# Optimization experiments

Hardware: AMD Instinct MI355X
Metric: run time of the kernel (lower is better)

Reference implementation:

```python
import jax, jax.numpy as jnp
import numpy as np

N = 40000   # nodes
E = 640000  # edges
D = 128     # hidden_dim
EPS = 1e-5  # LayerNorm eps


def setup_inputs() -> dict:
    key = jax.random.key(0)
    ks = jax.random.split(key, 18)
    s = 0.02
    inp = {
        "h": jax.random.normal(ks[0], (N, D), jnp.float32),
        "x": jax.random.normal(ks[1], (N, 3), jnp.float32),
        "edge_index": jax.random.randint(ks[2], (2, E), 0, N, jnp.int64 if jax.config.jax_enable_x64 else jnp.int32),
        "vel": jax.random.normal(ks[3], (N, 3), jnp.float32),
        # phi_e: Linear(2D+1 -> D), SiLU, Linear(D -> D), SiLU
        "We1": jax.random.normal(ks[4], (2 * D + 1, D), jnp.float32) * s,
        "be1": jnp.zeros((D,), jnp.float32),
        "We2": jax.random.normal(ks[5], (D, D), jnp.float32) * s,
        "be2": jnp.zeros((D,), jnp.float32),
        # phi_x: Linear(D -> D), SiLU, Linear(D -> 1)
        "Wx1": jax.random.normal(ks[6], (D, D), jnp.float32) * s,
        "bx1": jnp.zeros((D,), jnp.float32),
        "Wx2": jax.random.normal(ks[7], (D, 1), jnp.float32) * s,
        "bx2": jnp.zeros((1,), jnp.float32),
        # phi_h: Linear(2D -> D), SiLU, Linear(D -> D)
        "Wh1": jax.random.normal(ks[8], (2 * D, D), jnp.float32) * s,
        "bh1": jnp.zeros((D,), jnp.float32),
        "Wh2": jax.random.normal(ks[9], (D, D), jnp.float32) * s,
        "bh2": jnp.zeros((D,), jnp.float32),
        # LayerNorm
        "gamma": jnp.ones((D,), jnp.float32),
        "beta": jnp.zeros((D,), jnp.float32),
    }
    return inp


def reference(h, x, edge_index, vel,
              We1, be1, We2, be2,
              Wx1, bx1, Wx2, bx2,
              Wh1, bh1, Wh2, bh2,
              gamma, beta):
    src, dst = edge_index[0], edge_index[1]
    rel = x[src] - x[dst]                                  # [E,3]
    dist2 = jnp.sum(rel * rel, axis=-1, keepdims=True)     # [E,1]
    # note: original also computes dist/r_hat and vel[src] but never uses them

    # phi_e on edge features
    e_in = jnp.concatenate([h[src], h[dst], dist2], axis=-1)   # [E,2D+1]
    m = jax.nn.silu(e_in @ We1 + be1)
    m = jax.nn.silu(m @ We2 + be2)                             # [E,D]

    # coordinate update: scatter_mean of rel * phi_x(m) over dst
    coord_w = jax.nn.silu(m @ Wx1 + bx1) @ Wx2 + bx2           # [E,1]
    num = jax.ops.segment_sum(rel * coord_w, dst, num_segments=N)  # [N,3]
    cnt = jax.ops.segment_sum(jnp.ones((E, 1), x.dtype), dst, num_segments=N)
    x_new = x + num / jnp.maximum(cnt, 1.0)

    # node update: scatter_add of messages then phi_h + residual + LayerNorm
    agg = jax.ops.segment_sum(m, dst, num_segments=N)          # [N,D]
    upd = jax.nn.silu(jnp.concatenate([h, agg], axis=-1) @ Wh1 + bh1) @ Wh2 + bh2
    hn = h + upd
    mu = jnp.mean(hn, axis=-1, keepdims=True)
    var = jnp.var(hn, axis=-1, keepdims=True)
    h_out = (hn - mu) / jnp.sqrt(var + EPS) * gamma + beta
    return h_out, x_new
```

## Files before the change

kernel.cpp:

```cpp
#include <hip/hip_runtime.h>
#include <hip/hip_fp16.h>

#define NN 40000
#define NE 640000
#define DD 128
#define NW (NE/64)

typedef _Float16 half8 __attribute__((ext_vector_type(8)));
typedef float f32x4 __attribute__((ext_vector_type(4)));

__device__ __forceinline__ float silu_f(float x){
  return x * __builtin_amdgcn_rcpf(1.f + __expf(-x));
}

__device__ __forceinline__ half8 cvt_h8(float4 a, float4 b){
  half8 r;
  r[0]=(_Float16)a.x; r[1]=(_Float16)a.y; r[2]=(_Float16)a.z; r[3]=(_Float16)a.w;
  r[4]=(_Float16)b.x; r[5]=(_Float16)b.y; r[6]=(_Float16)b.z; r[7]=(_Float16)b.w;
  return r;
}

__device__ __forceinline__ void atom_pk_f16(_Float16* p, unsigned v){
  asm volatile("global_atomic_pk_add_f16 %0, %1, off" :: "v"(p), "v"(v));
}

__global__ void k_hist(const int* __restrict__ ei, int* __restrict__ counts,
                       uint4* __restrict__ aggz){
  int e = blockIdx.x*256 + threadIdx.x;
  if (e < NE){
    atomicAdd(&counts[ei[NE + e]], 1);
    aggz[e] = make_uint4(0,0,0,0);
  }
}

__global__ __launch_bounds__(1024)
void k_scanA(const int* __restrict__ counts, int* __restrict__ woff,
             int* __restrict__ bsum){
  __shared__ int wsum[16];
  const int tid = threadIdx.x, lane = tid & 63, wv = tid >> 6;
  int i = blockIdx.x*1024 + tid;
  int v = (i < NN) ? counts[i] : 0;
  int s = v;
  #pragma unroll
  for (int d = 1; d < 64; d <<= 1){
    int t = __shfl_up(s, d, 64);
    if (lane >= d) s += t;
  }
  if (lane == 63) wsum[wv] = s;
  __syncthreads();
  if (tid < 16){
    int t = wsum[tid];
    #pragma unroll
    for (int d = 1; d < 16; d <<= 1){
      int u = __shfl_up(t, d, 64);
      if (tid >= d) t += u;
    }
    wsum[tid] = t;
  }
  __syncthreads();
  int wbase = (wv == 0) ? 0 : wsum[wv-1];
  if (i < NN) woff[i] = wbase + s - v;
  if (tid == 1023) bsum[blockIdx.x] = wbase + s;
}

__global__ __launch_bounds__(1024)
void k_scanC(int* __restrict__ woff, const int* __restrict__ bsum){
  const int lane = threadIdx.x & 63;
  int v = (lane < 40) ? bsum[lane] : 0;
  int s = v;
  #pragma unroll
  for (int d = 1; d < 64; d <<= 1){
    int t = __shfl_up(s, d, 64);
    if (lane >= d) s += t;
  }
  int boff = (blockIdx.x == 0) ? 0 : __shfl(s, blockIdx.x - 1, 64);
  int i = blockIdx.x*1024 + threadIdx.x;
  if (i < NN) woff[i] += boff;
}

__global__ void k_wt(const float* __restrict__ We1, const float* __restrict__ Wh1,
                     const float* __restrict__ Wh2,
                     _Float16* __restrict__ We1t, _Float16* __restrict__ Wh1t,
                     _Float16* __restrict__ Wh2t, int* __restrict__ counts){
  int i = blockIdx.x*256 + threadIdx.x;
  if (i < 128*256){
    int ch = i >> 8, k = i & 255;
    We1t[i] = (_Float16)We1[k*128 + ch];
    Wh1t[i] = (_Float16)Wh1[k*128 + ch];
  }
  if (i < 128*128){
    int ch = i >> 7, k = i & 127;
    Wh2t[i] = (_Float16)Wh2[k*128 + ch];
  }
  for (int c = i; c < NN; c += 32768) counts[c] = 0;
}

__global__ __launch_bounds__(256)
void k_scatgpre(const int* __restrict__ ei, int* __restrict__ woff,
                unsigned* __restrict__ sdp,
                const float* __restrict__ h, const _Float16* __restrict__ We1t,
                const float* __restrict__ be1,
                _Float16* __restrict__ g1, _Float16* __restrict__ g2)
{
  if (blockIdx.x < NE/256){
    int e = blockIdx.x*256 + threadIdx.x;
    int s = ei[e];
    int d = ei[NE + e];
    int p = atomicAdd(&woff[d], 1);
    sdp[p] = ((unsigned)s << 16) | (unsigned)d;
    return;
  }
  const int b = blockIdx.x - NE/256;
  const int tid = threadIdx.x, lane = tid & 63, w = tid >> 6;
  const int q = lane & 15, g = lane >> 4;
  const int base = (b*4 + w) * 16;
  float be1r[8];
  #pragma unroll
  for (int nt=0; nt<8; nt++) be1r[nt] = be1[nt*16+q];

  half8 a[4];
  #pragma unroll
  for (int kk=0; kk<4; kk++){
    const float* rp = h + (size_t)(base+q)*DD + kk*32 + g*8;
    a[kk] = cvt_h8(*(const float4*)rp, *(const float4*)(rp+4));
  }
  f32x4 ac1[8] = {}, ac2[8] = {};
  #pragma unroll
  for (int kk=0; kk<4; kk++){
    #pragma unroll
    for (int nt=0; nt<8; nt++){
      half8 b1 = *(const half8*)&We1t[(nt*16+q)*256 + kk*32 + g*8];
      half8 b2 = *(const half8*)&We1t[(nt*16+q)*256 + 128 + kk*32 + g*8];
      ac1[nt] = __builtin_amdgcn_mfma_f32_16x16x32_f16(a[kk], b1, ac1[nt], 0,0,0);
      ac2[nt] = __builtin_amdgcn_mfma_f32_16x16x32_f16(a[kk], b2, ac2[nt], 0,0,0);
    }
  }
  #pragma unroll
  for (int r=0;r<4;r++){
    int node = base + 4*g + r;
    #pragma unroll
    for (int nt=0; nt<8; nt++){
      g1[(size_t)node*DD + nt*16+q] = (_Float16)(ac1[nt][r] + be1r[nt]);
      g2[(size_t)node*DD + nt*16+q] = (_Float16)ac2[nt][r];
    }
  }
}

__global__ __launch_bounds__(768, 3)
void egnn_edge(const _Float16* __restrict__ g1, const _Float16* __restrict__ g2,
               const float* __restrict__ x,
               const unsigned* __restrict__ sdp,
               const float* __restrict__ We1,
               const float* __restrict__ We2, const float* __restrict__ be2,
               const float* __restrict__ Wx1, const float* __restrict__ bx1,
               const float* __restrict__ Wx2, const float* __restrict__ bx2,
               _Float16* __restrict__ agg, float* __restrict__ cwb)
{
  __shared__ __align__(16) _Float16 W2t[128*128];
  __shared__ __align__(16) _Float16 Wxt[128*128];
  __shared__ __align__(16) _Float16 mbuf[12][16*128];
  __shared__ __align__(16) _Float16 w1l_lds[128];

  const int tid = threadIdx.x;
  for (int i = tid; i < 128*128; i += 768){
    int ch = i & 127, k = i >> 7;
    int sw = (ch & 15) << 3;
    W2t[ch*128 + (k ^ sw)] = (_Float16)We2[k*128 + ch];
    Wxt[ch*128 + (k ^ sw)] = (_Float16)Wx1[k*128 + ch];
  }
  if (tid < 128) w1l_lds[tid] = (_Float16)We1[256*128 + tid];
  const int lane = tid & 63;
  const int w    = tid >> 6;
  const int q    = lane & 15;
  const int g    = lane >> 4;
  float be2r[8], bx1r[8], wx2r[8];
  #pragma unroll
  for (int nt = 0; nt < 8; nt++){
    int ch = nt*16 + q;
    be2r[nt] = be2[ch];
    bx1r[nt] = bx1[ch];
    wx2r[nt] = Wx2[ch];
  }
  const float bx2s = bx2[0];
  _Float16* mb = mbuf[w];
  __syncthreads();

  const int gw = blockIdx.x*12 + w;
  if (gw >= NW) return;

  half8 w1l_h[4];
  #pragma unroll
  for (int kk=0; kk<4; kk++)
    w1l_h[kk] = *(const half8*)&w1l_lds[kk*32 + g*8];

  const unsigned sv = sdp[gw*64 + lane];
  const int esrc = (int)(sv >> 16);
  const int edst = (int)(sv & 0xffffu);
  float r0 = x[esrc*3+0] - x[edst*3+0];
  float r1 = x[esrc*3+1] - x[edst*3+1];
  float r2 = x[esrc*3+2] - x[edst*3+2];
  float d2 = r0*r0 + r1*r1 + r2*r2;

  const int first_dst = __shfl(edst, 0, 64);
  const int last_dst  = __shfl(edst, 63, 64);
  const bool prev_spill = (gw > 0)    && ((int)(sdp[gw*64 - 1] & 0xffffu) == first_dst);
  const bool next_spill = (gw < NW-1) && ((int)(sdp[gw*64 + 64] & 0xffffu) == last_dst);

  int srcq[4], dstq[4];
  __half2 d2h[4];
  #pragma unroll
  for (int mt=0; mt<4; mt++){
    srcq[mt] = __shfl(esrc, mt*16 + q, 64);
    dstq[mt] = __shfl(edst, mt*16 + q, 64);
    d2h[mt]  = __float2half2_rn(__shfl(d2, mt*16 + q, 64));
  }
  const __half2 one2 = __float2half2_rn(1.f);

  float fa0 = 0.f, fa1 = 0.f;
  int   fdprev = first_dst;
  bool  seg_first = true;

  uint4 pa1[4], pa2[4], pb1[4], pb2[4];
  #pragma unroll
  for (int kk=0; kk<4; kk++){
    pa1[kk] = *(const uint4*)(g1 + (size_t)srcq[0]*DD + kk*32 + g*8);
    pa2[kk] = *(const uint4*)(g2 + (size_t)dstq[0]*DD + kk*32 + g*8);
  }

  #pragma unroll
  for (int mt=0; mt<4; mt++){
    uint4 (&cu1)[4] = (mt&1) ? pb1 : pa1;
    uint4 (&cu2)[4] = (mt&1) ? pb2 : pa2;
    uint4 (&nu1)[4] = (mt&1) ? pa1 : pb1;
    uint4 (&nu2)[4] = (mt&1) ? pa2 : pb2;
    if (mt < 3){
      #pragma unroll
      for (int kk=0; kk<4; kk++){
        nu1[kk] = *(const uint4*)(g1 + (size_t)srcq[mt+1]*DD + kk*32 + g*8);
        nu2[kk] = *(const uint4*)(g2 + (size_t)dstq[mt+1]*DD + kk*32 + g*8);
      }
    }

    half8 a[4];
    #pragma unroll
    for (int kk=0; kk<4; kk++){
      uint4 w4 = __builtin_bit_cast(uint4, w1l_h[kk]);
      unsigned uu1[4] = {cu1[kk].x, cu1[kk].y, cu1[kk].z, cu1[kk].w};
      unsigned uu2[4] = {cu2[kk].x, cu2[kk].y, cu2[kk].z, cu2[kk].w};
      unsigned ww[4]  = {w4.x, w4.y, w4.z, w4.w};
      unsigned zz[4];
      #pragma unroll
      for (int p2=0; p2<4; p2++){
        __half2 z = __hadd2(__builtin_bit_cast(__half2, uu1[p2]),
                            __builtin_bit_cast(__half2, uu2[p2]));
        z = __hfma2(d2h[mt], __builtin_bit_cast(__half2, ww[p2]), z);
        __half2 e   = h2exp(__hneg2(z));
        __half2 den = __hadd2(e, one2);
        __half2 m   = __hmul2(z, h2rcp(den));
        zz[p2] = __builtin_bit_cast(unsigned, m);
      }
      uint4 t; t.x = zz[0]; t.y = zz[1]; t.z = zz[2]; t.w = zz[3];
      a[kk] = __builtin_bit_cast(half8, t);
    }

    f32x4 acc2[8] = {};
    #pragma unroll
    for (int kk=0; kk<4; kk++){
      #pragma unroll
      for (int nt=0; nt<8; nt++){
        half8 b = *(const half8*)&W2t[(nt*16+q)*128 + ((kk*32+g*8) ^ (q<<3))];
        acc2[nt] = __builtin_amdgcn_mfma_f32_16x16x32_f16(a[kk], b, acc2[nt], 0,0,0);
      }
    }
    #pragma unroll
    for (int nt=0; nt<8; nt++){
      #pragma unroll
      for (int r=0;r<4;r++){
        float s = silu_f(acc2[nt][r] + be2r[nt]);
        int el = 4*g + r;
        mb[el*128 + ((nt*16+q) ^ (el<<3))] = (_Float16)s;
      }
    }
    f32x4 acc3[8] = {};
    #pragma unroll
    for (int kk=0; kk<4; kk++){
      half8 am = *(const half8*)&mb[q*128 + ((kk*32+g*8) ^ (q<<3))];
      #pragma unroll
      for (int nt=0; nt<8; nt++){
        half8 b = *(const half8*)&Wxt[(nt*16+q)*128 + ((kk*32+g*8) ^ (q<<3))];
        acc3[nt] = __builtin_amdgcn_mfma_f32_16x16x32_f16(am, b, acc3[nt], 0,0,0);
      }
    }
    float part[4] = {0.f,0.f,0.f,0.f};
    #pragma unroll
    for (int nt=0; nt<8; nt++){
      #pragma unroll
      for (int r=0;r<4;r++)
        part[r] += silu_f(acc3[nt][r] + bx1r[nt]) * wx2r[nt];
    }
    #pragma unroll
    for (int m=1; m<16; m<<=1){
      #pragma unroll
      for (int r=0;r<4;r++) part[r] += __shfl_xor(part[r], m, 64);
    }
    {
      float cw = part[0];
      if (q==1) cw = part[1]; else if (q==2) cw = part[2]; else if (q==3) cw = part[3];
      if (q < 4) cwb[gw*64 + mt*16 + 4*g + q] = cw + bx2s;
    }
    {
      unsigned mv[16];
      #pragma unroll
      for (int e2=0; e2<16; e2++)
        mv[e2] = *(const unsigned*)&mb[e2*128 + ((2*lane) ^ (e2<<3))];
      int dv[16];
      #pragma unroll
      for (int e2=0; e2<16; e2++) dv[e2] = __shfl(edst, mt*16 + e2, 64);
      #pragma unroll
      for (int e2=0; e2<16; e2++){
        if (dv[e2] != fdprev){
          __half2 hv; hv.x = __float2half(fa0); hv.y = __float2half(fa1);
          _Float16* p = agg + (size_t)fdprev*DD + 2*lane;
          if (seg_first && prev_spill) atom_pk_f16(p, __builtin_bit_cast(unsigned, hv));
          else                         *(__half2*)p = hv;
          fa0 = 0.f; fa1 = 0.f; fdprev = dv[e2]; seg_first = false;
        }
        __half2 mvv = __builtin_bit_cast(__half2, mv[e2]);
        fa0 += __half2float(mvv.x);
        fa1 += __half2float(mvv.y);
      }
    }
  }
  {
    __half2 hv; hv.x = __float2half(fa0); hv.y = __float2half(fa1);
    _Float16* p = agg + (size_t)fdprev*DD + 2*lane;
    if ((seg_first && prev_spill) || next_spill) atom_pk_f16(p, __builtin_bit_cast(unsigned, hv));
    else                                         *(__half2*)p = hv;
  }
}

__global__ __launch_bounds__(256)
void k_nodecoord(const float* __restrict__ h, const _Float16* __restrict__ agg,
                 const _Float16* __restrict__ Wh1t, const _Float16* __restrict__ Wh2t,
                 const float* __restrict__ bh1, const float* __restrict__ bh2,
                 const float* __restrict__ gam, const float* __restrict__ bet,
                 const float* __restrict__ x, const float* __restrict__ cwb,
                 const unsigned* __restrict__ sdp, const int* __restrict__ counts,
                 const int* __restrict__ woff,
                 float* __restrict__ hout, float* __restrict__ xout)
{
  __shared__ __align__(16) _Float16 mbuf[4][16*128];
  const int tid = threadIdx.x, lane = tid & 63, w = tid >> 6;

  if (blockIdx.x >= NN/64){
    const int bidx = blockIdx.x - NN/64;
    const int sub = lane >> 4, j0 = lane & 15;
    const int n = (bidx*4 + w)*4 + sub;
    if (n >= NN) return;
    const int cnt = counts[n];
    const int s = woff[n] - cnt;
    float xd0 = x[n*3+0], xd1 = x[n*3+1], xd2 = x[n*3+2];
    float s0=0.f, s1=0.f, s2=0.f;
    for (int j = j0; j < cnt; j += 16){
      int e = s + j;
      float cw = cwb[e];
      int src = (int)(sdp[e] >> 16);
      s0 += (x[src*3+0]-xd0)*cw;
      s1 += (x[src*3+1]-xd1)*cw;
      s2 += (x[src*3+2]-xd2)*cw;
    }
    #pragma unroll
    for (int m=1; m<16; m<<=1){
      s0 += __shfl_xor(s0, m, 64);
      s1 += __shfl_xor(s1, m, 64);
      s2 += __shfl_xor(s2, m, 64);
    }
    if (j0 == 0){
      float inv = __builtin_amdgcn_rcpf((float)(cnt > 1 ? cnt : 1));
      xout[n*3+0] = xd0 + s0*inv;
      xout[n*3+1] = xd1 + s1*inv;
      xout[n*3+2] = xd2 + s2*inv;
    }
    return;
  }

  const int q = lane & 15, g = lane >> 4;
  const int base = (blockIdx.x*4 + w) * 16;
  float bh1r[8], bh2r[8], gr[8], br[8];
  #pragma unroll
  for (int nt=0; nt<8; nt++){
    int ch = nt*16+q;
    bh1r[nt]=bh1[ch]; bh2r[nt]=bh2[ch]; gr[nt]=gam[ch]; br[nt]=bet[ch];
  }
  _Float16* mb = mbuf[w];

  f32x4 ac1[8] = {};
  #pragma unroll
  for (int kk=0; kk<8; kk++){
    half8 a;
    if (kk < 4){
      const float* rp = h + (size_t)(base+q)*DD + kk*32 + g*8;
      a = cvt_h8(*(const float4*)rp, *(const float4*)(rp+4));
    } else {
      a = *(const half8*)(agg + (size_t)(base+q)*DD + (kk-4)*32 + g*8);
    }
    #pragma unroll
    for (int nt=0; nt<8; nt++){
      half8 b = *(const half8*)&Wh1t[(nt*16+q)*256 + kk*32 + g*8];
      ac1[nt] = __builtin_amdgcn_mfma_f32_16x16x32_f16(a, b, ac1[nt], 0,0,0);
    }
  }
  #pragma unroll
  for (int nt=0; nt<8; nt++){
    #pragma unroll
    for (int r=0;r<4;r++){
      float s = silu_f(ac1[nt][r] + bh1r[nt]);
      int el = 4*g + r;
      mb[el*128 + ((nt*16+q) ^ (el<<3))] = (_Float16)s;
    }
  }
  f32x4 ac2[8] = {};
  #pragma unroll
  for (int kk=0; kk<4; kk++){
    half8 am = *(const half8*)&mb[q*128 + ((kk*32+g*8) ^ (q<<3))];
    #pragma unroll
    for (int nt=0; nt<8; nt++){
      half8 b = *(const half8*)&Wh2t[(nt*16+q)*128 + kk*32 + g*8];
      ac2[nt] = __builtin_amdgcn_mfma_f32_16x16x32_f16(am, b, ac2[nt], 0,0,0);
    }
  }
  #pragma unroll
  for (int r=0;r<4;r++){
    int node = base + 4*g + r;
    float hv[8]; float s1=0.f, s2=0.f;
    #pragma unroll
    for (int nt=0; nt<8; nt++){
      float v = ac2[nt][r] + bh2r[nt] + h[(size_t)node*DD + nt*16 + q];
      hv[nt]=v; s1 += v; s2 += v*v;
    }
    #pragma unroll
    for (int m=1;m<16;m<<=1){ s1 += __shfl_xor(s1,m,64); s2 += __shfl_xor(s2,m,64); }
    float mu  = s1 * (1.f/128.f);
    float var = s2 * (1.f/128.f) - mu*mu;
    float rs  = rsqrtf(var + 1e-5f);
    #pragma unroll
    for (int nt=0; nt<8; nt++)
      hout[(size_t)node*DD + nt*16 + q] = (hv[nt]-mu)*rs*gr[nt] + br[nt];
  }
}

extern "C" void kernel_launch(void* const* d_in, const int* in_sizes, int n_in,
                              void* d_out, int out_size, void* d_ws, size_t ws_size,
                              hipStream_t stream){
  const float* h   = (const float*)d_in[0];
  const float* x   = (const float*)d_in[1];
  const int*   ei  = (const int*)d_in[2];
  const float* We1 = (const float*)d_in[4];
  const float* be1 = (const float*)d_in[5];
  const float* We2 = (const float*)d_in[6];
  const float* be2 = (const float*)d_in[7];
  const float* Wx1 = (const float*)d_in[8];
  const float* bx1 = (const float*)d_in[9];
  const float* Wx2 = (const float*)d_in[10];
  const float* bx2 = (const float*)d_in[11];
  const float* Wh1 = (const float*)d_in[12];
  const float* bh1 = (const float*)d_in[13];
  const float* Wh2 = (const float*)d_in[14];
  const float* bh2 = (const float*)d_in[15];
  const float* gam = (const float*)d_in[16];
  const float* bet = (const float*)d_in[17];

  float* hout = (float*)d_out;
  float* xout = hout + (size_t)NN*DD;

  char* p = (char*)d_ws;
  _Float16* agg  = (_Float16*)p;  p += (size_t)NN*DD*2;
  _Float16* g1   = (_Float16*)p;  p += (size_t)NN*DD*2;
  _Float16* g2   = (_Float16*)p;  p += (size_t)NN*DD*2;
  int* counts    = (int*)p;       p += (size_t)NN*4;
  int* woff      = (int*)p;       p += (size_t)NN*4;
  unsigned* sdp  = (unsigned*)p;  p += (size_t)NE*4;
  float* cwb     = (float*)p;     p += (size_t)NE*4;
  _Float16* We1t = (_Float16*)p;  p += (size_t)128*256*2;
  _Float16* Wh1t = (_Float16*)p;  p += (size_t)128*256*2;
  _Float16* Wh2t = (_Float16*)p;  p += (size_t)128*128*2;
  int* bsum      = (int*)p;       p += 64*4;

  k_wt<<<128, 256, 0, stream>>>(We1, Wh1, Wh2, We1t, Wh1t, Wh2t, counts);
  k_hist<<<(NE+255)/256, 256, 0, stream>>>(ei, counts, (uint4*)agg);
  k_scanA<<<(NN+1023)/1024, 1024, 0, stream>>>(counts, woff, bsum);
  k_scanC<<<(NN+1023)/1024, 1024, 0, stream>>>(woff, bsum);
  k_scatgpre<<<NE/256 + NN/64, 256, 0, stream>>>(ei, woff, sdp, h, We1t, be1, g1, g2);
  egnn_edge<<<(NW + 11)/12, 768, 0, stream>>>(g1, g2, x, sdp, We1,
                                              We2, be2, Wx1, bx1, Wx2, bx2,
                                              agg, cwb);
  k_nodecoord<<<NN/64 + NN/16, 256, 0, stream>>>(h, agg, Wh1t, Wh2t, bh1, bh2,
                                                 gam, bet, x, cwb, sdp, counts,
                                                 woff, hout, xout);
}
```

Baseline: 332.8 us.

## Read fp16 edge MLP weights from global memory instead of LDS

The edge kernel no longer transposes We2 and Wx1 into LDS per block. The weight-prep kernel now writes pre-transposed fp16 copies to global memory once, and the edge kernel loads its MFMA B operands straight from global/L2. Dropping 64KB of LDS per block, and raising the launch-bounds occupancy hint from 3 to 6, should allow more resident blocks and remove the per-block conversion prologue. The trade-off is that every weight fragment load now goes through the vector memory/cache path rather than LDS, and the higher occupancy hint may force register spills.

```diff
diff --git a/kernel.cpp b/kernel.cpp
--- a/kernel.cpp
+++ b/kernel.cpp
@@ -79,9 +79,11 @@
 }
 
 __global__ void k_wt(const float* __restrict__ We1, const float* __restrict__ Wh1,
-                     const float* __restrict__ Wh2,
+                     const float* __restrict__ Wh2, const float* __restrict__ We2,
+                     const float* __restrict__ Wx1,
                      _Float16* __restrict__ We1t, _Float16* __restrict__ Wh1t,
-                     _Float16* __restrict__ Wh2t, int* __restrict__ counts){
+                     _Float16* __restrict__ Wh2t, _Float16* __restrict__ We2t,
+                     _Float16* __restrict__ Wxtg, int* __restrict__ counts){
   int i = blockIdx.x*256 + threadIdx.x;
   if (i < 128*256){
     int ch = i >> 8, k = i & 255;
@@ -91,6 +93,8 @@
   if (i < 128*128){
     int ch = i >> 7, k = i & 127;
     Wh2t[i] = (_Float16)Wh2[k*128 + ch];
+    We2t[i] = (_Float16)We2[k*128 + ch];
+    Wxtg[i] = (_Float16)Wx1[k*128 + ch];
   }
   for (int c = i; c < NN; c += 32768) counts[c] = 0;
 }
@@ -146,28 +150,20 @@
   }
 }
 
-__global__ __launch_bounds__(768, 3)
+__global__ __launch_bounds__(768, 6)
 void egnn_edge(const _Float16* __restrict__ g1, const _Float16* __restrict__ g2,
                const float* __restrict__ x,
                const unsigned* __restrict__ sdp,
                const float* __restrict__ We1,
-               const float* __restrict__ We2, const float* __restrict__ be2,
-               const float* __restrict__ Wx1, const float* __restrict__ bx1,
+               const _Float16* __restrict__ We2t, const float* __restrict__ be2,
+               const _Float16* __restrict__ Wxtg, const float* __restrict__ bx1,
                const float* __restrict__ Wx2, const float* __restrict__ bx2,
                _Float16* __restrict__ agg, float* __restrict__ cwb)
 {
-  __shared__ __align__(16) _Float16 W2t[128*128];
-  __shared__ __align__(16) _Float16 Wxt[128*128];
   __shared__ __align__(16) _Float16 mbuf[12][16*128];
   __shared__ __align__(16) _Float16 w1l_lds[128];
 
   const int tid = threadIdx.x;
-  for (int i = tid; i < 128*128; i += 768){
-    int ch = i & 127, k = i >> 7;
-    int sw = (ch & 15) << 3;
-    W2t[ch*128 + (k ^ sw)] = (_Float16)We2[k*128 + ch];
-    Wxt[ch*128 + (k ^ sw)] = (_Float16)Wx1[k*128 + ch];
-  }
   if (tid < 128) w1l_lds[tid] = (_Float16)We1[256*128 + tid];
   const int lane = tid & 63;
   const int w    = tid >> 6;
@@ -268,7 +264,7 @@
     for (int kk=0; kk<4; kk++){
       #pragma unroll
       for (int nt=0; nt<8; nt++){
-        half8 b = *(const half8*)&W2t[(nt*16+q)*128 + ((kk*32+g*8) ^ (q<<3))];
+        half8 b = *(const half8*)&We2t[(nt*16+q)*128 + kk*32 + g*8];
         acc2[nt] = __builtin_amdgcn_mfma_f32_16x16x32_f16(a[kk], b, acc2[nt], 0,0,0);
       }
     }
@@ -287,7 +283,7 @@
       half8 am = *(const half8*)&mb[q*128 + ((kk*32+g*8) ^ (q<<3))];
       #pragma unroll
       for (int nt=0; nt<8; nt++){
-        half8 b = *(const half8*)&Wxt[(nt*16+q)*128 + ((kk*32+g*8) ^ (q<<3))];
+        half8 b = *(const half8*)&Wxtg[(nt*16+q)*128 + kk*32 + g*8];
         acc3[nt] = __builtin_amdgcn_mfma_f32_16x16x32_f16(am, b, acc3[nt], 0,0,0);
       }
     }
@@ -484,15 +480,18 @@
   _Float16* We1t = (_Float16*)p;  p += (size_t)128*256*2;
   _Float16* Wh1t = (_Float16*)p;  p += (size_t)128*256*2;
   _Float16* Wh2t = (_Float16*)p;  p += (size_t)128*128*2;
+  _Float16* We2t = (_Float16*)p;  p += (size_t)128*128*2;
+  _Float16* Wxtg = (_Float16*)p;  p += (size_t)128*128*2;
   int* bsum      = (int*)p;       p += 64*4;
 
-  k_wt<<<128, 256, 0, stream>>>(We1, Wh1, Wh2, We1t, Wh1t, Wh2t, counts);
+  k_wt<<<128, 256, 0, stream>>>(We1, Wh1, Wh2, We2, Wx1,
+                                We1t, Wh1t, Wh2t, We2t, Wxtg, counts);
   k_hist<<<(NE+255)/256, 256, 0, stream>>>(ei, counts, (uint4*)agg);
   k_scanA<<<(NN+1023)/1024, 1024, 0, stream>>>(counts, woff, bsum);
   k_scanC<<<(NN+1023)/1024, 1024, 0, stream>>>(woff, bsum);
   k_scatgpre<<<NE/256 + NN/64, 256, 0, stream>>>(ei, woff, sdp, h, We1t, be1, g1, g2);
   egnn_edge<<<(NW + 11)/12, 768, 0, stream>>>(g1, g2, x, sdp, We1,
-                                              We2, be2, Wx1, bx1, Wx2, bx2,
+                                              We2t, be2, Wxtg, bx1, Wx2, bx2,
                                               agg, cwb);
   k_nodecoord<<<NN/64 + NN/16, 256, 0, stream>>>(h, agg, Wh1t, Wh2t, bh1, bh2,
                                                  gam, bet, x, cwb, sdp, counts,
```

After: 968.5 us. 2.91x slower.
